# Kernel tuning notes

Measured on AMD Instinct MI355X. Metric: run time of the kernel, lower is better.

The kernel has to match this reference:

```python
import jax, jax.numpy as jnp
import numpy as np

B, C, H, W = 4, 2048, 14, 14
N_CLS, WORD_D, INT_D = 80, 300, 1024


def setup_inputs() -> dict:
    key = jax.random.key(0)
    ks = jax.random.split(key, 8)
    s = lambda fan_in: 1.0 / np.sqrt(fan_in)
    return {
        "img_feature_map": jax.random.normal(ks[0], (B, C, H, W), jnp.float32),
        "word_features": jax.random.normal(ks[1], (N_CLS, WORD_D), jnp.float32),
        "fc1_w": jax.random.uniform(ks[2], (INT_D, C), jnp.float32, -s(C), s(C)),
        "fc2_w": jax.random.uniform(ks[3], (INT_D, WORD_D), jnp.float32, -s(WORD_D), s(WORD_D)),
        "fc3_w": jax.random.uniform(ks[4], (INT_D, INT_D), jnp.float32, -s(INT_D), s(INT_D)),
        "fc3_b": jax.random.uniform(ks[5], (INT_D,), jnp.float32, -s(INT_D), s(INT_D)),
        "fc4_w": jax.random.uniform(ks[6], (1, INT_D), jnp.float32, -s(INT_D), s(INT_D)),
        "fc4_b": jax.random.uniform(ks[7], (1,), jnp.float32, -s(INT_D), s(INT_D)),
    }


def reference(img_feature_map, word_features, fc1_w, fc2_w, fc3_w, fc3_b, fc4_w, fc4_b):
    b, c, h, w = img_feature_map.shape
    n = word_features.shape[0]
    # [B,C,H,W] -> [B,H,W,C]
    x = jnp.transpose(img_feature_map, (0, 2, 3, 1))
    img_p = jnp.einsum('bhwc,dc->bhwd', x, fc1_w)            # [B,H,W,INT_D]
    word_p = word_features @ fc2_w.T                          # [N,INT_D]
    # broadcast product instead of .repeat(): [B,H,W,N,INT_D]
    feat = jnp.tanh(img_p[:, :, :, None, :] * word_p[None, None, None, :, :])
    feat = jnp.einsum('bhwnd,ed->bhwne', feat, fc3_w) + fc3_b
    coef = jnp.einsum('bhwnd,d->bhwn', feat, fc4_w[0]) + fc4_b[0]  # [B,H,W,N]
    # softmax over spatial positions per (batch, class)
    coef = jax.nn.softmax(coef.reshape(b, h * w, n), axis=1).reshape(b, h, w, n)
    # weighted spatial pooling: [B,N,C]
    return jnp.einsum('bhwn,bhwc->bnc', coef, x)
```

## Files before the change

kernel.cpp:

```cpp
#include <hip/hip_runtime.h>

typedef __attribute__((ext_vector_type(8))) short short8;
typedef __attribute__((ext_vector_type(4))) float f32x4;

#define B_   4
#define C_   2048
#define HW_  196
#define P_   784
#define NCLS 80
#define WD   300
#define ID   1024

#define WP_OFF    0
#define V_OFF     81920
#define BS_OFF    82944
#define IMGP_OFF  83968
#define LG_OFF    3295232
#define SM_OFF    3357952
#define ABF_BYTE  13682688
#define WBF_BYTE  16893952

__device__ __forceinline__ unsigned short f2bf(float x) {
    unsigned u = __float_as_uint(x);
    return (unsigned short)((u + 0x7FFFu + ((u >> 16) & 1u)) >> 16);
}

typedef __attribute__((ext_vector_type(4))) unsigned short u16x4;
__global__ __launch_bounds__(256) void k_cvtW(const float* __restrict__ w,
                                              unsigned short* __restrict__ wbf) {
    int i = (blockIdx.x * 256 + threadIdx.x) * 4;
    float4 v = *(const float4*)(w + i);
    u16x4 r = {f2bf(v.x), f2bf(v.y), f2bf(v.z), f2bf(v.w)};
    *(u16x4*)(wbf + i) = r;
}

__global__ __launch_bounds__(256) void k_cvtA(const float* __restrict__ img,
                                              unsigned short* __restrict__ abf) {
    __shared__ unsigned short tile[HW_][65];
    int b = blockIdx.y, c0 = blockIdx.x * 64, t = threadIdx.x;
    for (int idx = t; idx < 64 * HW_; idx += 256) {
        int c = idx / HW_, hw = idx - c * HW_;
        tile[hw][c] = f2bf(img[((size_t)b * C_ + c0 + c) * HW_ + hw]);
    }
    __syncthreads();
    for (int idx = t; idx < 64 * HW_; idx += 256) {
        int hw = idx >> 6, c = idx & 63;
        abf[((size_t)b * HW_ + hw) * C_ + c0 + c] = tile[hw][c];
    }
}

__global__ __launch_bounds__(256) void k_wordp(const float* __restrict__ wf,
                                               const float* __restrict__ fc2w,
                                               float* __restrict__ wp) {
    int idx = blockIdx.x * 256 + threadIdx.x;
    int n = idx >> 10, d = idx & 1023;
    const float4* a = (const float4*)(wf + n * WD);
    const float4* b = (const float4*)(fc2w + d * WD);
    float s = 0.f;
    #pragma unroll 5
    for (int k = 0; k < WD / 4; ++k) {
        float4 x = a[k], y = b[k];
        s += x.x * y.x + x.y * y.y + x.z * y.z + x.w * y.w;
    }
    wp[idx] = s;
}

__global__ __launch_bounds__(256) void k_v(const float* __restrict__ fc3w,
                                           const float* __restrict__ fc4w,
                                           float* __restrict__ v) {
    int d  = blockIdx.x * 256 + threadIdx.x;
    int e0 = blockIdx.y * 64;
    float s = 0.f;
    #pragma unroll 8
    for (int e = e0; e < e0 + 64; ++e) s += fc4w[e] * fc3w[e * ID + d];
    atomicAdd(&v[d], s);
}

__global__ __launch_bounds__(256) void k_bs(const float* __restrict__ fc3b,
                                            const float* __restrict__ fc4w,
                                            const float* __restrict__ fc4b,
                                            float* __restrict__ bs) {
    __shared__ float red[256];
    int t = threadIdx.x;
    float s = 0.f;
    for (int i = t; i < ID; i += 256) s += fc3b[i] * fc4w[i];
    red[t] = s; __syncthreads();
    for (int o = 128; o > 0; o >>= 1) { if (t < o) red[t] += red[t + o]; __syncthreads(); }
    if (t == 0) bs[0] = red[0] + fc4b[0];
}

#define LDT 72
__global__ __launch_bounds__(256) void k_fc1(const unsigned short* __restrict__ Abf,
                                             const unsigned short* __restrict__ Wbf,
                                             float* __restrict__ imgp4) {
    __shared__ unsigned short As[2][64 * LDT];
    __shared__ unsigned short Bs[2][64 * LDT];
    int t = threadIdx.x;
    int bx = blockIdx.x, by = blockIdx.y, bz = blockIdx.z;
    int w = t >> 6, l = t & 63;
    int lr = l & 15, lhi = l >> 4;
    int row = t >> 2, cq = (t & 3) * 16;

    int pA = bx * 64 + row;
    int pAc = pA < P_ ? pA : P_ - 1;
    const unsigned short* aBase = Abf + (size_t)pAc * C_ + bz * 512 + cq;
    const unsigned short* bBase = Wbf + (size_t)(by * 64 + row) * C_ + bz * 512 + cq;

    short8 ra0, ra1, rb0, rb1;
    f32x4 acc[4];
    #pragma unroll
    for (int j = 0; j < 4; ++j) acc[j] = (f32x4){0.f, 0.f, 0.f, 0.f};

    #define LOADR(kc) { \
        const short8* ap = (const short8*)(aBase + (kc) * 64); \
        const short8* bp = (const short8*)(bBase + (kc) * 64); \
        ra0 = ap[0]; ra1 = ap[1]; rb0 = bp[0]; rb1 = bp[1]; }
    #define WRITES(buf) { \
        *(short8*)&As[buf][row * LDT + cq]     = ra0; \
        *(short8*)&As[buf][row * LDT + cq + 8] = ra1; \
        *(short8*)&Bs[buf][row * LDT + cq]     = rb0; \
        *(short8*)&Bs[buf][row * LDT + cq + 8] = rb1; }

    LOADR(0);
    WRITES(0);
    __syncthreads();

    for (int kc = 0; kc < 8; ++kc) {
        int cur = kc & 1;
        if (kc < 7) LOADR(kc + 1);
        #pragma unroll
        for (int kk = 0; kk < 2; ++kk) {
            short8 af = *reinterpret_cast<const short8*>(
                &As[cur][(w * 16 + lr) * LDT + kk * 32 + lhi * 8]);
            #pragma unroll
            for (int j = 0; j < 4; ++j) {
                short8 bfr = *reinterpret_cast<const short8*>(
                    &Bs[cur][(j * 16 + lr) * LDT + kk * 32 + lhi * 8]);
                acc[j] = __builtin_amdgcn_mfma_f32_16x16x32_bf16(af, bfr, acc[j], 0, 0, 0);
            }
        }
        if (kc < 7) WRITES(cur ^ 1);
        __syncthreads();
    }
    #undef LOADR
    #undef WRITES

    float* outp = imgp4 + (size_t)bz * (P_ * ID);
    int prow = bx * 64 + w * 16 + lhi * 4;
    int dcol = by * 64 + lr;
    #pragma unroll
    for (int j = 0; j < 4; ++j)
        #pragma unroll
        for (int i = 0; i < 4; ++i)
            if (prow + i < P_) outp[(size_t)(prow + i) * ID + dcol + j * 16] = acc[j][i];
}

__global__ __launch_bounds__(256) void k_logits(const float* __restrict__ imgp4,
                                                const float* __restrict__ wp,
                                                const float* __restrict__ v,
                                                const float* __restrict__ bs,
                                                float* __restrict__ lg) {
    int p = blockIdx.x;
    int wv = threadIdx.x >> 6, lane = threadIdx.x & 63;
    const int S4 = P_ * ID / 4;
    const f32x4* a0 = (const f32x4*)(imgp4 + (size_t)p * ID) + lane * 4;
    const f32x4* v4 = (const f32x4*)v + lane * 4;
    const float K2 = 2.8853900817779268f;
    f32x4 a2[4], nv2[4];
    float sv = 0.f;
    #pragma unroll
    for (int q = 0; q < 4; ++q) {
        f32x4 aq = a0[q] + a0[S4 + q] + a0[2 * S4 + q] + a0[3 * S4 + q];
        f32x4 vq = v4[q];
        a2[q] = aq * K2;
        nv2[q] = vq * -2.0f;
        sv += vq.x + vq.y + vq.z + vq.w;
    }
    float bsv = bs[0];
    #pragma unroll 2
    for (int nn = 0; nn < 20; ++nn) {
        int n = wv * 20 + nn;
        const f32x4* w4 = (const f32x4*)(wp + (size_t)n * ID) + lane * 4;
        float s = sv;
        #pragma unroll
        for (int q = 0; q < 4; ++q) {
            f32x4 wq = w4[q];
            float e0 = __builtin_amdgcn_exp2f(a2[q].x * wq.x);
            float e1 = __builtin_amdgcn_exp2f(a2[q].y * wq.y);
            float e2 = __builtin_amdgcn_exp2f(a2[q].z * wq.z);
            float e3 = __builtin_amdgcn_exp2f(a2[q].w * wq.w);
            s += nv2[q].x * __builtin_amdgcn_rcpf(e0 + 1.f);
            s += nv2[q].y * __builtin_amdgcn_rcpf(e1 + 1.f);
            s += nv2[q].z * __builtin_amdgcn_rcpf(e2 + 1.f);
            s += nv2[q].w * __builtin_amdgcn_rcpf(e3 + 1.f);
        }
        #pragma unroll
        for (int off = 32; off > 0; off >>= 1) s += __shfl_xor(s, off, 64);
        if (lane == 0) lg[p * NCLS + n] = s + bsv;
    }
}

__global__ __launch_bounds__(256) void k_softmax(const float* __restrict__ lg,
                                                 float* __restrict__ sm) {
    __shared__ float red[256];
    int b = blockIdx.x, n = blockIdx.y, t = threadIdx.x;
    float x = (t < HW_) ? lg[(b * HW_ + t) * NCLS + n] : -1e30f;
    red[t] = x; __syncthreads();
    for (int o = 128; o > 0; o >>= 1) { if (t < o) red[t] = fmaxf(red[t], red[t + o]); __syncthreads(); }
    float mx = red[0]; __syncthreads();
    float e = (t < HW_) ? __expf(x - mx) : 0.f;
    red[t] = e; __syncthreads();
    for (int o = 128; o > 0; o >>= 1) { if (t < o) red[t] += red[t + o]; __syncthreads(); }
    float inv = __builtin_amdgcn_rcpf(red[0]);
    if (t < HW_) sm[(b * NCLS + n) * HW_ + t] = e * inv;
}

__global__ __launch_bounds__(256) void k_pool(const float* __restrict__ sm,
                                              const float* __restrict__ img,
                                              float* __restrict__ out) {
    __shared__ float smt[16 * HW_];
    int cb = blockIdx.x, nt = blockIdx.y, b = blockIdx.z, t = threadIdx.x;
    for (int i = t; i < 16 * HW_; i += 256)
        smt[i] = sm[(b * NCLS + nt * 16) * HW_ + i];
    __syncthreads();
    int c = cb * 256 + t;
    const float* row = img + (b * C_ + c) * HW_;
    float acc[16] = {};
    for (int h4 = 0; h4 < HW_ / 4; ++h4) {
        float4 iv = *(const float4*)(row + h4 * 4);
        #pragma unroll
        for (int nl = 0; nl < 16; ++nl) {
            float4 s4 = *(const float4*)&smt[nl * HW_ + h4 * 4];
            acc[nl] += iv.x * s4.x + iv.y * s4.y + iv.z * s4.z + iv.w * s4.w;
        }
    }
    #pragma unroll
    for (int nl = 0; nl < 16; ++nl)
        out[(b * NCLS + nt * 16 + nl) * C_ + c] = acc[nl];
}

extern "C" void kernel_launch(void* const* d_in, const int* in_sizes, int n_in,
                              void* d_out, int out_size, void* d_ws, size_t ws_size,
                              hipStream_t stream) {
    const float* img  = (const float*)d_in[0];
    const float* wf   = (const float*)d_in[1];
    const float* fc1w = (const float*)d_in[2];
    const float* fc2w = (const float*)d_in[3];
    const float* fc3w = (const float*)d_in[4];
    const float* fc3b = (const float*)d_in[5];
    const float* fc4w = (const float*)d_in[6];
    const float* fc4b = (const float*)d_in[7];
    float* out = (float*)d_out;
    float* ws  = (float*)d_ws;

    float* wp    = ws + WP_OFF;
    float* v     = ws + V_OFF;
    float* bs    = ws + BS_OFF;
    float* imgp4 = ws + IMGP_OFF;
    float* lg    = ws + LG_OFF;
    float* sm    = ws + SM_OFF;
    unsigned short* Abf = (unsigned short*)((char*)d_ws + ABF_BYTE);
    unsigned short* Wbf = (unsigned short*)((char*)d_ws + WBF_BYTE);

    hipMemsetAsync(v, 0, ID * sizeof(float), stream);

    k_cvtW   <<<dim3(2048),      256, 0, stream>>>(fc1w, Wbf);
    k_cvtA   <<<dim3(32, 4),     256, 0, stream>>>(img, Abf);
    k_wordp  <<<dim3(320),       256, 0, stream>>>(wf, fc2w, wp);
    k_v      <<<dim3(4, 16),     256, 0, stream>>>(fc3w, fc4w, v);
    k_bs     <<<dim3(1),         256, 0, stream>>>(fc3b, fc4w, fc4b, bs);
    k_fc1    <<<dim3(13, 16, 4), 256, 0, stream>>>(Abf, Wbf, imgp4);
    k_logits <<<dim3(784),       256, 0, stream>>>(imgp4, wp, v, bs, lg);
    k_softmax<<<dim3(4, 80),     256, 0, stream>>>(lg, sm);
    k_pool   <<<dim3(8, 5, 4),   256, 0, stream>>>(sm, img, out);
}
```

Measured before the change: 188.9 us.

## Merge prep kernels, fold softmax into pool, stage word projections in LDS

Folds the four preprocessing kernels (fc1 weight conversion, image transpose/convert, word projection, fc3·fc4 vector) into a single block-indexed launch. The memset and atomic reduction for v become per-chunk partials, and one fc1 block reduces them and computes the bias scalar. Softmax moves into the pooling kernel, and the logits kernel handles four positions per block, sharing word-projection rows staged through LDS. This removes several launches and intermediate round trips. The cost is divergent block roles and one block in fc1 doing extra serial work.

```diff
diff --git a/kernel.cpp b/kernel.cpp
--- a/kernel.cpp
+++ b/kernel.cpp
@@ -2,6 +2,7 @@
 
 typedef __attribute__((ext_vector_type(8))) short short8;
 typedef __attribute__((ext_vector_type(4))) float f32x4;
+typedef __attribute__((ext_vector_type(4))) unsigned short u16x4;
 
 #define B_   4
 #define C_   2048
@@ -16,83 +17,81 @@
 #define BS_OFF    82944
 #define IMGP_OFF  83968
 #define LG_OFF    3295232
-#define SM_OFF    3357952
-#define ABF_BYTE  13682688
-#define WBF_BYTE  16893952
+#define VPART_OFF 3357952
+#define ABF_BYTE  13748224
+#define WBF_BYTE  16959488
 
 __device__ __forceinline__ unsigned short f2bf(float x) {
     unsigned u = __float_as_uint(x);
     return (unsigned short)((u + 0x7FFFu + ((u >> 16) & 1u)) >> 16);
 }
 
-typedef __attribute__((ext_vector_type(4))) unsigned short u16x4;
-__global__ __launch_bounds__(256) void k_cvtW(const float* __restrict__ w,
-                                              unsigned short* __restrict__ wbf) {
-    int i = (blockIdx.x * 256 + threadIdx.x) * 4;
-    float4 v = *(const float4*)(w + i);
-    u16x4 r = {f2bf(v.x), f2bf(v.y), f2bf(v.z), f2bf(v.w)};
-    *(u16x4*)(wbf + i) = r;
-}
-
-__global__ __launch_bounds__(256) void k_cvtA(const float* __restrict__ img,
-                                              unsigned short* __restrict__ abf) {
-    __shared__ unsigned short tile[HW_][65];
-    int b = blockIdx.y, c0 = blockIdx.x * 64, t = threadIdx.x;
-    for (int idx = t; idx < 64 * HW_; idx += 256) {
-        int c = idx / HW_, hw = idx - c * HW_;
-        tile[hw][c] = f2bf(img[((size_t)b * C_ + c0 + c) * HW_ + hw]);
-    }
-    __syncthreads();
-    for (int idx = t; idx < 64 * HW_; idx += 256) {
-        int hw = idx >> 6, c = idx & 63;
-        abf[((size_t)b * HW_ + hw) * C_ + c0 + c] = tile[hw][c];
-    }
-}
-
-__global__ __launch_bounds__(256) void k_wordp(const float* __restrict__ wf,
-                                               const float* __restrict__ fc2w,
-                                               float* __restrict__ wp) {
-    int idx = blockIdx.x * 256 + threadIdx.x;
-    int n = idx >> 10, d = idx & 1023;
-    const float4* a = (const float4*)(wf + n * WD);
-    const float4* b = (const float4*)(fc2w + d * WD);
-    float s = 0.f;
-    #pragma unroll 5
-    for (int k = 0; k < WD / 4; ++k) {
-        float4 x = a[k], y = b[k];
-        s += x.x * y.x + x.y * y.y + x.z * y.z + x.w * y.w;
-    }
-    wp[idx] = s;
-}
-
-__global__ __launch_bounds__(256) void k_v(const float* __restrict__ fc3w,
-                                           const float* __restrict__ fc4w,
-                                           float* __restrict__ v) {
-    int d  = blockIdx.x * 256 + threadIdx.x;
-    int e0 = blockIdx.y * 64;
-    float s = 0.f;
-    #pragma unroll 8
-    for (int e = e0; e < e0 + 64; ++e) s += fc4w[e] * fc3w[e * ID + d];
-    atomicAdd(&v[d], s);
-}
-
-__global__ __launch_bounds__(256) void k_bs(const float* __restrict__ fc3b,
-                                            const float* __restrict__ fc4w,
-                                            const float* __restrict__ fc4b,
-                                            float* __restrict__ bs) {
-    __shared__ float red[256];
-    int t = threadIdx.x;
-    float s = 0.f;
-    for (int i = t; i < ID; i += 256) s += fc3b[i] * fc4w[i];
-    red[t] = s; __syncthreads();
-    for (int o = 128; o > 0; o >>= 1) { if (t < o) red[t] += red[t + o]; __syncthreads(); }
-    if (t == 0) bs[0] = red[0] + fc4b[0];
+__global__ __launch_bounds__(256) void k_prep(const float* __restrict__ img,
+                                              const float* __restrict__ wf,
+                                              const float* __restrict__ fc1w,
+                                              const float* __restrict__ fc2w,
+                                              const float* __restrict__ fc3w,
+                                              const float* __restrict__ fc4w,
+                                              unsigned short* __restrict__ abf,
+                                              unsigned short* __restrict__ wbf,
+                                              float* __restrict__ wp,
+                                              float* __restrict__ vpart) {
+    __shared__ unsigned short tile[HW_][68];
+    int bid = blockIdx.x, t = threadIdx.x;
+    if (bid < 320) {
+        int idx = bid * 256 + t;
+        int n = idx >> 10, d = idx & 1023;
+        const float4* a = (const float4*)(wf + n * WD);
+        const float4* b = (const float4*)(fc2w + d * WD);
+        float s = 0.f;
+        #pragma unroll 5
+        for (int k = 0; k < WD / 4; ++k) {
+            float4 x = a[k], y = b[k];
+            s += x.x * y.x + x.y * y.y + x.z * y.z + x.w * y.w;
+        }
+        wp[idx] = s;
+    } else if (bid < 832) {
+        size_t base = (size_t)(bid - 320) * 4096 + (size_t)t * 16;
+        #pragma unroll
+        for (int j = 0; j < 4; ++j) {
+            float4 v4 = *(const float4*)(fc1w + base + j * 4);
+            u16x4 r = {f2bf(v4.x), f2bf(v4.y), f2bf(v4.z), f2bf(v4.w)};
+            *(u16x4*)(wbf + base + j * 4) = r;
+        }
+    } else if (bid < 960) {
+        int bc = bid - 832;
+        int c0 = (bc >> 2) * 64, b = bc & 3;
+        for (int idx = t; idx < 64 * HW_; idx += 256) {
+            int c = idx / HW_, hw = idx - c * HW_;
+            tile[hw][c] = f2bf(img[((size_t)b * C_ + c0 + c) * HW_ + hw]);
+        }
+        __syncthreads();
+        for (int q = t; q < 16 * HW_; q += 256) {
+            int hw = q >> 4, c4 = (q & 15) * 4;
+            u16x4 r = *(const u16x4*)&tile[hw][c4];
+            *(u16x4*)(abf + ((size_t)b * HW_ + hw) * C_ + c0 + c4) = r;
+        }
+    } else {
+        int idx = bid - 960;
+        int ec = idx >> 2;
+        int d = (idx & 3) * 256 + t;
+        float s = 0.f;
+        #pragma unroll 8
+        for (int e = ec * 64; e < ec * 64 + 64; ++e) s += fc4w[e] * fc3w[e * ID + d];
+        vpart[ec * ID + d] = s;
+    }
 }
 
 #define LDT 72
 __global__ __launch_bounds__(256) void k_fc1(const unsigned short* __restrict__ Abf,
                                              const unsigned short* __restrict__ Wbf,
-                                             float* __restrict__ imgp4) {
+                                             const float* __restrict__ fc3b,
+                                             const float* __restrict__ fc4w,
+                                             const float* __restrict__ fc4b,
+                                             const float* __restrict__ vpart,
+                                             float* __restrict__ imgp4,
+                                             float* __restrict__ v,
+                                             float* __restrict__ bs) {
     __shared__ unsigned short As[2][64 * LDT];
     __shared__ unsigned short Bs[2][64 * LDT];
     int t = threadIdx.x;
@@ -153,6 +152,22 @@
         #pragma unroll
         for (int i = 0; i < 4; ++i)
             if (prow + i < P_) outp[(size_t)(prow + i) * ID + dcol + j * 16] = acc[j][i];
+
+    if (bx == 0 && by == 0 && bz == 0) {
+        for (int d = t; d < ID; d += 256) {
+            float s = 0.f;
+            #pragma unroll
+            for (int k = 0; k < 16; ++k) s += vpart[k * ID + d];
+            v[d] = s;
+        }
+        float s = 0.f;
+        for (int i = t; i < ID; i += 256) s += fc3b[i] * fc4w[i];
+        __syncthreads();
+        float* red = (float*)&As[0][0];
+        red[t] = s; __syncthreads();
+        for (int o = 128; o > 0; o >>= 1) { if (t < o) red[t] += red[t + o]; __syncthreads(); }
+        if (t == 0) bs[0] = red[0] + fc4b[0];
+    }
 }
 
 __global__ __launch_bounds__(256) void k_logits(const float* __restrict__ imgp4,
@@ -160,71 +175,96 @@
                                                 const float* __restrict__ v,
                                                 const float* __restrict__ bs,
                                                 float* __restrict__ lg) {
-    int p = blockIdx.x;
-    int wv = threadIdx.x >> 6, lane = threadIdx.x & 63;
-    const int S4 = P_ * ID / 4;
-    const f32x4* a0 = (const f32x4*)(imgp4 + (size_t)p * ID) + lane * 4;
-    const f32x4* v4 = (const f32x4*)v + lane * 4;
+    __shared__ float wpl[8 * ID];
+    int bx = blockIdx.x, by = blockIdx.y;
+    int t = threadIdx.x, wv = t >> 6, lane = t & 63;
+    int p = bx * 4 + wv;
+    const int S = P_ * ID;
+    const float* ap = imgp4 + (size_t)p * ID;
     const float K2 = 2.8853900817779268f;
     f32x4 a2[4], nv2[4];
     float sv = 0.f;
     #pragma unroll
     for (int q = 0; q < 4; ++q) {
-        f32x4 aq = a0[q] + a0[S4 + q] + a0[2 * S4 + q] + a0[3 * S4 + q];
-        f32x4 vq = v4[q];
+        int d = q * 256 + lane * 4;
+        f32x4 aq = *(const f32x4*)(ap + d);
+        aq += *(const f32x4*)(ap + S + d);
+        aq += *(const f32x4*)(ap + 2 * S + d);
+        aq += *(const f32x4*)(ap + 3 * S + d);
+        f32x4 vq = *(const f32x4*)(v + d);
         a2[q] = aq * K2;
         nv2[q] = vq * -2.0f;
         sv += vq.x + vq.y + vq.z + vq.w;
     }
     float bsv = bs[0];
-    #pragma unroll 2
-    for (int nn = 0; nn < 20; ++nn) {
-        int n = wv * 20 + nn;
-        const f32x4* w4 = (const f32x4*)(wp + (size_t)n * ID) + lane * 4;
-        float s = sv;
-        #pragma unroll
-        for (int q = 0; q < 4; ++q) {
-            f32x4 wq = w4[q];
-            float e0 = __builtin_amdgcn_exp2f(a2[q].x * wq.x);
-            float e1 = __builtin_amdgcn_exp2f(a2[q].y * wq.y);
-            float e2 = __builtin_amdgcn_exp2f(a2[q].z * wq.z);
-            float e3 = __builtin_amdgcn_exp2f(a2[q].w * wq.w);
-            s += nv2[q].x * __builtin_amdgcn_rcpf(e0 + 1.f);
-            s += nv2[q].y * __builtin_amdgcn_rcpf(e1 + 1.f);
-            s += nv2[q].z * __builtin_amdgcn_rcpf(e2 + 1.f);
-            s += nv2[q].w * __builtin_amdgcn_rcpf(e3 + 1.f);
-        }
-        #pragma unroll
-        for (int off = 32; off > 0; off >>= 1) s += __shfl_xor(s, off, 64);
-        if (lane == 0) lg[p * NCLS + n] = s + bsv;
-    }
-}
-
-__global__ __launch_bounds__(256) void k_softmax(const float* __restrict__ lg,
-                                                 float* __restrict__ sm) {
-    __shared__ float red[256];
-    int b = blockIdx.x, n = blockIdx.y, t = threadIdx.x;
-    float x = (t < HW_) ? lg[(b * HW_ + t) * NCLS + n] : -1e30f;
-    red[t] = x; __syncthreads();
-    for (int o = 128; o > 0; o >>= 1) { if (t < o) red[t] = fmaxf(red[t], red[t + o]); __syncthreads(); }
-    float mx = red[0]; __syncthreads();
-    float e = (t < HW_) ? __expf(x - mx) : 0.f;
-    red[t] = e; __syncthreads();
-    for (int o = 128; o > 0; o >>= 1) { if (t < o) red[t] += red[t + o]; __syncthreads(); }
-    float inv = __builtin_amdgcn_rcpf(red[0]);
-    if (t < HW_) sm[(b * NCLS + n) * HW_ + t] = e * inv;
-}
-
-__global__ __launch_bounds__(256) void k_pool(const float* __restrict__ sm,
+    int n0 = by * 40;
+    for (int ch = 0; ch < 5; ++ch) {
+        __syncthreads();
+        #pragma unroll
+        for (int j = 0; j < 8; ++j) {
+            int flat = t * 32 + j * 4;
+            *(f32x4*)(wpl + flat) =
+                *(const f32x4*)(wp + (size_t)(n0 + ch * 8 + (flat >> 10)) * ID + (flat & 1023));
+        }
+        __syncthreads();
+        #pragma unroll
+        for (int r = 0; r < 8; ++r) {
+            float s = sv;
+            #pragma unroll
+            for (int q = 0; q < 4; ++q) {
+                f32x4 wq = *(const f32x4*)(wpl + r * ID + q * 256 + lane * 4);
+                float e0 = __builtin_amdgcn_exp2f(a2[q].x * wq.x);
+                float e1 = __builtin_amdgcn_exp2f(a2[q].y * wq.y);
+                float e2 = __builtin_amdgcn_exp2f(a2[q].z * wq.z);
+                float e3 = __builtin_amdgcn_exp2f(a2[q].w * wq.w);
+                s += nv2[q].x * __builtin_amdgcn_rcpf(e0 + 1.f);
+                s += nv2[q].y * __builtin_amdgcn_rcpf(e1 + 1.f);
+                s += nv2[q].z * __builtin_amdgcn_rcpf(e2 + 1.f);
+                s += nv2[q].w * __builtin_amdgcn_rcpf(e3 + 1.f);
+            }
+            #pragma unroll
+            for (int off = 32; off > 0; off >>= 1) s += __shfl_xor(s, off, 64);
+            if (lane == 0) lg[p * NCLS + n0 + ch * 8 + r] = s + bsv;
+        }
+    }
+}
+
+__global__ __launch_bounds__(256) void k_pool(const float* __restrict__ lg,
                                               const float* __restrict__ img,
                                               float* __restrict__ out) {
     __shared__ float smt[16 * HW_];
     int cb = blockIdx.x, nt = blockIdx.y, b = blockIdx.z, t = threadIdx.x;
-    for (int i = t; i < 16 * HW_; i += 256)
-        smt[i] = sm[(b * NCLS + nt * 16) * HW_ + i];
+    int n_l = t >> 4, seg = t & 15;
+    int n = nt * 16 + n_l;
+    float xr[13];
+    float mx = -1e30f;
+    #pragma unroll
+    for (int j = 0; j < 13; ++j) {
+        int hw = seg + j * 16;
+        float x = (hw < HW_) ? lg[(size_t)(b * HW_ + hw) * NCLS + n] : -1e30f;
+        xr[j] = x; mx = fmaxf(mx, x);
+    }
+    #pragma unroll
+    for (int o = 8; o > 0; o >>= 1) mx = fmaxf(mx, __shfl_xor(mx, o, 16));
+    float sum = 0.f;
+    #pragma unroll
+    for (int j = 0; j < 13; ++j) {
+        int hw = seg + j * 16;
+        float e = (hw < HW_) ? __expf(xr[j] - mx) : 0.f;
+        xr[j] = e; sum += e;
+    }
+    #pragma unroll
+    for (int o = 8; o > 0; o >>= 1) sum += __shfl_xor(sum, o, 16);
+    float inv = __builtin_amdgcn_rcpf(sum);
+    #pragma unroll
+    for (int j = 0; j < 13; ++j) {
+        int hw = seg + j * 16;
+        if (hw < HW_) smt[n_l * HW_ + hw] = xr[j] * inv;
+    }
     __syncthreads();
+
     int c = cb * 256 + t;
-    const float* row = img + (b * C_ + c) * HW_;
+    const float* row = img + ((size_t)b * C_ + c) * HW_;
     float acc[16] = {};
     for (int h4 = 0; h4 < HW_ / 4; ++h4) {
         float4 iv = *(const float4*)(row + h4 * 4);
@@ -236,7 +276,7 @@
     }
     #pragma unroll
     for (int nl = 0; nl < 16; ++nl)
-        out[(b * NCLS + nt * 16 + nl) * C_ + c] = acc[nl];
+        out[((size_t)b * NCLS + nt * 16 + nl) * C_ + c] = acc[nl];
 }
 
 extern "C" void kernel_launch(void* const* d_in, const int* in_sizes, int n_in,
@@ -258,19 +298,14 @@
     float* bs    = ws + BS_OFF;
     float* imgp4 = ws + IMGP_OFF;
     float* lg    = ws + LG_OFF;
-    float* sm    = ws + SM_OFF;
+    float* vpart = ws + VPART_OFF;
     unsigned short* Abf = (unsigned short*)((char*)d_ws + ABF_BYTE);
     unsigned short* Wbf = (unsigned short*)((char*)d_ws + WBF_BYTE);
 
-    hipMemsetAsync(v, 0, ID * sizeof(float), stream);
-
-    k_cvtW   <<<dim3(2048),      256, 0, stream>>>(fc1w, Wbf);
-    k_cvtA   <<<dim3(32, 4),     256, 0, stream>>>(img, Abf);
-    k_wordp  <<<dim3(320),       256, 0, stream>>>(wf, fc2w, wp);
-    k_v      <<<dim3(4, 16),     256, 0, stream>>>(fc3w, fc4w, v);
-    k_bs     <<<dim3(1),         256, 0, stream>>>(fc3b, fc4w, fc4b, bs);
-    k_fc1    <<<dim3(13, 16, 4), 256, 0, stream>>>(Abf, Wbf, imgp4);
-    k_logits <<<dim3(784),       256, 0, stream>>>(imgp4, wp, v, bs, lg);
-    k_softmax<<<dim3(4, 80),     256, 0, stream>>>(lg, sm);
-    k_pool   <<<dim3(8, 5, 4),   256, 0, stream>>>(sm, img, out);
-}
+    k_prep   <<<dim3(1024),      256, 0, stream>>>(img, wf, fc1w, fc2w, fc3w, fc4w,
+                                                   Abf, Wbf, wp, vpart);
+    k_fc1    <<<dim3(13, 16, 4), 256, 0, stream>>>(Abf, Wbf, fc3b, fc4w, fc4b, vpart,
+                                                   imgp4, v, bs);
+    k_logits <<<dim3(196, 2),    256, 0, stream>>>(imgp4, wp, v, bs, lg);
+    k_pool   <<<dim3(8, 5, 4),   256, 0, stream>>>(lg, img, out);
+}
```

Measured after the change: 169.5 us. 10.3% less time.
